# Kernel tuning notes

Measured on AMD Instinct MI355X. Metric: run time of the kernel, lower is better.

The kernel has to match this reference:

```python
import jax, jax.numpy as jnp
import numpy as np

DIM = 1024
NH = 16
HD = DIM // NH  # 64
NT = max(1, int(NH * 0.25))  # 4 time heads
NS = NH - NT                 # 12 space heads
SCALE = HD ** (-0.5)


def setup_inputs() -> dict:
    key = jax.random.key(0)
    ks = jax.random.split(key, 8)
    B, T = 2, 2048
    init = 0.02
    return {
        "x": jax.random.normal(ks[0], (B, T, DIM), dtype=jnp.float32),
        # weights stored as (in, out); torch Linear y = x @ W.T is equivalent
        "Wqt": jax.random.normal(ks[1], (DIM, NT * HD), dtype=jnp.float32) * init,
        "Wkt": jax.random.normal(ks[2], (DIM, NT * HD), dtype=jnp.float32) * init,
        "Wqs": jax.random.normal(ks[3], (DIM, NS * HD), dtype=jnp.float32) * init,
        "Wks": jax.random.normal(ks[4], (DIM, NS * HD), dtype=jnp.float32) * init,
        "Wv": jax.random.normal(ks[5], (DIM, DIM), dtype=jnp.float32) * init,
        "Wout": jax.random.normal(ks[6], (DIM, DIM), dtype=jnp.float32) * init,
        "bout": jnp.zeros((DIM,), dtype=jnp.float32),
        "w_sigma": jnp.zeros((1,), dtype=jnp.float32),
    }


def reference(x, Wqt, Wkt, Wqs, Wks, Wv, Wout, bout, w_sigma):
    B, T, D = x.shape
    Qt = (x @ Wqt).reshape(B, T, NT, HD)
    Kt = (x @ Wkt).reshape(B, T, NT, HD)
    Qs = (x @ Wqs).reshape(B, T, NS, HD)
    Ks = (x @ Wks).reshape(B, T, NS, HD)
    st = jnp.einsum('bthd,bshd->bths', Qt, Kt)  # [B,T,NT,T]
    ss = jnp.einsum('bthd,bshd->bths', Qs, Ks)  # [B,T,NS,T]
    sig = jax.nn.sigmoid(w_sigma)  # shape (1,), broadcasts
    score = jnp.concatenate([-sig * st, ss], axis=2) * SCALE  # [B,T,NH,T]
    attn = jax.nn.softmax(score, axis=-1)
    V = (x @ Wv).reshape(B, T, NH, HD)
    ctx = jnp.einsum('bths,bshd->bthd', attn, V).reshape(B, T, D)
    return ctx @ Wout + bout
```

## Files before the change

### kernel.cpp

```cpp
#include <hip/hip_runtime.h>
#include <hip/hip_bf16.h>

typedef __bf16 bf16_t;
typedef __bf16 bf16x4 __attribute__((ext_vector_type(4)));
typedef __bf16 bf16x8 __attribute__((ext_vector_type(8)));
typedef float  f32x4  __attribute__((ext_vector_type(4)));

#define DIM     1024
#define NHEAD   16
#define HDIM    64
#define NTIME   4
#define TSEQ    2048
#define NBATCH  2
#define SCALE_F 0.125f
#define LOG2E   1.4426950408889634f

#define GLL(gp, lp) __builtin_amdgcn_global_load_lds( \
    (const __attribute__((address_space(1))) unsigned int*)(const void*)(gp), \
    (__attribute__((address_space(3))) unsigned int*)(void*)(lp), 16, 0, 0)

#define OFF_WQKVT 0UL
#define OFF_WOUTT (OFF_WQKVT + 3072UL*1024UL*2UL)
#define OFF_Q     (OFF_WOUTT + 1024UL*1024UL*2UL)
#define OFF_K     (OFF_Q  + 2UL*16UL*2048UL*64UL*2UL)
#define OFF_VT    (OFF_K  + 2UL*16UL*2048UL*64UL*2UL)
#define OFF_CTX   (OFF_VT + 2UL*16UL*2048UL*64UL*2UL)

__global__ void prep_all(const float* __restrict__ x,
                         const float* __restrict__ Wqt, const float* __restrict__ Wkt,
                         const float* __restrict__ Wqs, const float* __restrict__ Wks,
                         const float* __restrict__ Wv,  const float* __restrict__ Wout,
                         bf16_t* __restrict__ Xb, bf16_t* __restrict__ WqkvT,
                         bf16_t* __restrict__ WoutT) {
    __shared__ float T[64][65];
    const int bid = blockIdx.x;
    if (bid < 2048) {
        int i = bid * 256 + threadIdx.x;
        const float4* s = (const float4*)(x + (size_t)i * 8);
        float4 a = s[0], b2 = s[1];
        bf16x8 v;
        v[0] = (bf16_t)a.x;  v[1] = (bf16_t)a.y;  v[2] = (bf16_t)a.z;  v[3] = (bf16_t)a.w;
        v[4] = (bf16_t)b2.x; v[5] = (bf16_t)b2.y; v[6] = (bf16_t)b2.z; v[7] = (bf16_t)b2.w;
        *(bf16x8*)(Xb + (size_t)i * 8) = v;
        return;
    }
    const int tc = threadIdx.x & 63, tr = threadIdx.x >> 6;
    if (bid < 2816) {
        const int l = bid - 2048;
        const int n0 = (l % 48) * 64;
        const int k0 = (l / 48) * 64;
        const int region = n0 >> 10;
        const int cc = n0 & 1023;
        const int h = cc >> 6;
        const float* src; int ncols, col0;
        if (region == 2) { src = Wv; ncols = 1024; col0 = cc; }
        else if (h < NTIME) { src = (region == 0) ? Wqt : Wkt; ncols = NTIME * HDIM; col0 = h * HDIM; }
        else                { src = (region == 0) ? Wqs : Wks; ncols = (NHEAD - NTIME) * HDIM; col0 = (h - NTIME) * HDIM; }
#pragma unroll
        for (int i = 0; i < 16; ++i) {
            int kl = tr * 16 + i;
            T[kl][tc] = src[(size_t)(k0 + kl) * ncols + col0 + tc];
        }
        __syncthreads();
#pragma unroll
        for (int i = 0; i < 16; ++i) {
            int nl = tr * 16 + i;
            WqkvT[(size_t)(n0 + nl) * 1024 + k0 + tc] = (bf16_t)T[tc][nl];
        }
    } else {
        const int l = bid - 2816;
        const int n0 = (l % 16) * 64;
        const int k0 = (l / 16) * 64;
#pragma unroll
        for (int i = 0; i < 16; ++i) {
            int kl = tr * 16 + i;
            T[kl][tc] = Wout[(size_t)(k0 + kl) * 1024 + n0 + tc];
        }
        __syncthreads();
#pragma unroll
        for (int i = 0; i < 16; ++i) {
            int nl = tr * 16 + i;
            WoutT[(size_t)(n0 + nl) * 1024 + k0 + tc] = (bf16_t)T[tc][nl];
        }
    }
}

template<int MODE, int NB>
__global__ __launch_bounds__(256)
void gemm_bf16(const bf16_t* __restrict__ Ab, const bf16_t* __restrict__ Bt,
               bf16_t* __restrict__ Qb, bf16_t* __restrict__ Kb, bf16_t* __restrict__ Vt,
               float* __restrict__ Cout, const float* __restrict__ bias)
{
    __shared__ __align__(16) bf16_t As[128][64];
    __shared__ __align__(16) bf16_t Bs[128][64];

    const int cpx = gridDim.x >> 3;
    const int l = (blockIdx.x & 7) * cpx + (blockIdx.x >> 3);
    const int m0 = (l / NB) * 128, n0 = (l % NB) * 128;

    const int tid  = threadIdx.x;
    const int lane = tid & 63;
    const int wave = tid >> 6;
    const int wm = (wave >> 1) * 64, wn = (wave & 1) * 64;
    const int g = lane >> 4, lr = lane & 15;

    f32x4 acc[4][4];
#pragma unroll
    for (int i = 0; i < 4; ++i)
#pragma unroll
        for (int j = 0; j < 4; ++j) acc[i][j] = f32x4{0.f, 0.f, 0.f, 0.f};

    for (int k0 = 0; k0 < 1024; k0 += 64) {
        __syncthreads();
#pragma unroll
        for (int c = 0; c < 4; ++c) {
            int idx  = tid + c * 256;
            int row  = idx >> 3;
            int csrc = (idx & 7) ^ (row & 7);
            GLL(Ab + (size_t)(m0 + row) * 1024 + k0 + csrc * 8,
                (char*)&As[0][0] + (c * 256 + wave * 64) * 16);
            GLL(Bt + (size_t)(n0 + row) * 1024 + k0 + csrc * 8,
                (char*)&Bs[0][0] + (c * 256 + wave * 64) * 16);
        }
        __syncthreads();

#pragma unroll
        for (int kk = 0; kk < 2; ++kk) {
            bf16x8 afr[4], bfr[4];
#pragma unroll
            for (int f = 0; f < 4; ++f) {
                int ra = wm + f * 16 + lr;
                afr[f] = *(const bf16x8*)((const char*)&As[0][0] + ra * 128 + (((kk * 4 + g) ^ (ra & 7)) << 4));
                int rb = wn + f * 16 + lr;
                bfr[f] = *(const bf16x8*)((const char*)&Bs[0][0] + rb * 128 + (((kk * 4 + g) ^ (rb & 7)) << 4));
            }
#pragma unroll
            for (int fm = 0; fm < 4; ++fm)
#pragma unroll
                for (int fn = 0; fn < 4; ++fn)
                    acc[fm][fn] = __builtin_amdgcn_mfma_f32_16x16x32_bf16(bfr[fn], afr[fm], acc[fm][fn], 0, 0, 0);
        }
    }

    const int region = n0 >> 10;
#pragma unroll
    for (int fm = 0; fm < 4; ++fm) {
        const int m = m0 + wm + fm * 16 + lr;
        const int b = m >> 11, t = m & 2047;
        const int ts = (t & ~31) | (((t >> 2) & 3) << 3) | (((t >> 4) & 1) << 2) | (t & 3);
#pragma unroll
        for (int fn = 0; fn < 4; ++fn) {
            const int nb = n0 + wn + fn * 16 + g * 4;
            if constexpr (MODE == 1) {
                float4 bb = *(const float4*)(bias + nb);
                float4 v;
                v.x = acc[fm][fn][0] + bb.x;
                v.y = acc[fm][fn][1] + bb.y;
                v.z = acc[fm][fn][2] + bb.z;
                v.w = acc[fm][fn][3] + bb.w;
                *(float4*)(Cout + (size_t)m * DIM + nb) = v;
            } else {
                const int cc = nb & 1023;
                const int h = cc >> 6, d0 = cc & 63;
                const size_t bh = (size_t)(b * NHEAD + h);
                if (region == 2) {
#pragma unroll
                    for (int r = 0; r < 4; ++r)
                        Vt[(bh * HDIM + d0 + r) * TSEQ + ts] = (bf16_t)acc[fm][fn][r];
                } else {
                    bf16x4 w;
#pragma unroll
                    for (int r = 0; r < 4; ++r) w[r] = (bf16_t)acc[fm][fn][r];
                    bf16_t* dst = (region == 0) ? Qb : Kb;
                    *(bf16x4*)(dst + (bh * TSEQ + t) * HDIM + d0) = w;
                }
            }
        }
    }
}

__global__ __launch_bounds__(256, 2)
void attn_kernel(const bf16_t* __restrict__ Qb, const bf16_t* __restrict__ Kb,
                 const bf16_t* __restrict__ Vt, bf16_t* __restrict__ ctx,
                 const float* __restrict__ w_sigma)
{
    __shared__ __align__(16) bf16_t Ktile[4][64][64];
    __shared__ __align__(16) bf16_t Vtile[4][64][64];

    const int l    = ((blockIdx.x & 7) << 6) + (blockIdx.x >> 3);
    const int qc   = l & 15;
    const int bh   = l >> 4;
    const int h    = bh & 15;
    const int b    = bh >> 4;
    const int tid  = threadIdx.x;
    const int lane = tid & 63;
    const int wave = tid >> 6;
    const int g = lane >> 4, lr = lane & 15;
    const int q0 = qc * 128 + wave * 32;

    const float sig = 1.f / (1.f + __expf(-w_sigma[0]));
    const float fl2 = ((h < NTIME) ? (-sig * SCALE_F) : SCALE_F) * LOG2E;

    const bf16_t* Qp = Qb + (size_t)bh * TSEQ * HDIM;
    const bf16_t* Kp = Kb + (size_t)bh * TSEQ * HDIM;
    const bf16_t* Vp = Vt + (size_t)bh * HDIM * TSEQ;

    bf16x8 qa0 = *(const bf16x8*)(Qp + (size_t)(q0 + lr) * HDIM + g * 8);
    bf16x8 qa1 = *(const bf16x8*)(Qp + (size_t)(q0 + lr) * HDIM + 32 + g * 8);
    bf16x8 qb0 = *(const bf16x8*)(Qp + (size_t)(q0 + 16 + lr) * HDIM + g * 8);
    bf16x8 qb1 = *(const bf16x8*)(Qp + (size_t)(q0 + 16 + lr) * HDIM + 32 + g * 8);
#pragma unroll
    for (int e = 0; e < 8; ++e) {
        qa0[e] = (bf16_t)((float)qa0[e] * fl2);
        qa1[e] = (bf16_t)((float)qa1[e] * fl2);
        qb0[e] = (bf16_t)((float)qb0[e] * fl2);
        qb1[e] = (bf16_t)((float)qb1[e] * fl2);
    }

    f32x4 oA[4], oB[4];
#pragma unroll
    for (int n = 0; n < 4; ++n) { oA[n] = f32x4{0.f,0.f,0.f,0.f}; oB[n] = f32x4{0.f,0.f,0.f,0.f}; }
    float lpA = 0.f, lpB = 0.f;

    const int trow = tid >> 3;
    const int tcg  = tid & 7;

    auto stage = [&](int s0, int buf) {
#pragma unroll
        for (int j = 0; j < 2; ++j) {
            int kr = j * 32 + trow;
            GLL(Kp + (size_t)(s0 + kr) * HDIM + ((tcg ^ (kr & 7)) << 3),
                (char*)&Ktile[buf][0][0] + (j * 256 + wave * 64) * 16);
            int vr = j * 32 + trow;
            GLL(Vp + (size_t)vr * TSEQ + s0 + ((tcg ^ (vr & 7)) << 3),
                (char*)&Vtile[buf][0][0] + (j * 256 + wave * 64) * 16);
        }
    };

    auto compute = [&](const char* Kt, const char* Vc) {
        bf16x4 wA[4], wB[4];
        __builtin_amdgcn_s_setprio(1);
#pragma unroll
        for (int st = 0; st < 4; ++st) {
            const int srow = st * 16 + lr;
            const int rs7 = lr & 7;
            bf16x8 kb0 = *(const bf16x8*)(Kt + srow * 128 + ((g ^ rs7) << 4));
            bf16x8 kb1 = *(const bf16x8*)(Kt + srow * 128 + (((4 + g) ^ rs7) << 4));
            f32x4 zA = f32x4{0.f,0.f,0.f,0.f}, zB = f32x4{0.f,0.f,0.f,0.f};
            zA = __builtin_amdgcn_mfma_f32_16x16x32_bf16(kb0, qa0, zA, 0, 0, 0);
            zA = __builtin_amdgcn_mfma_f32_16x16x32_bf16(kb1, qa1, zA, 0, 0, 0);
            zB = __builtin_amdgcn_mfma_f32_16x16x32_bf16(kb0, qb0, zB, 0, 0, 0);
            zB = __builtin_amdgcn_mfma_f32_16x16x32_bf16(kb1, qb1, zB, 0, 0, 0);
            float a0 = __builtin_amdgcn_exp2f(zA[0]);
            float a1 = __builtin_amdgcn_exp2f(zA[1]);
            float a2 = __builtin_amdgcn_exp2f(zA[2]);
            float a3 = __builtin_amdgcn_exp2f(zA[3]);
            float b0 = __builtin_amdgcn_exp2f(zB[0]);
            float b1 = __builtin_amdgcn_exp2f(zB[1]);
            float b2 = __builtin_amdgcn_exp2f(zB[2]);
            float b3 = __builtin_amdgcn_exp2f(zB[3]);
            wA[st][0] = (bf16_t)a0; wA[st][1] = (bf16_t)a1; wA[st][2] = (bf16_t)a2; wA[st][3] = (bf16_t)a3;
            wB[st][0] = (bf16_t)b0; wB[st][1] = (bf16_t)b1; wB[st][2] = (bf16_t)b2; wB[st][3] = (bf16_t)b3;
            lpA += (a0 + a1) + (a2 + a3);
            lpB += (b0 + b1) + (b2 + b3);
        }
        __builtin_amdgcn_s_setprio(0);

        __builtin_amdgcn_s_setprio(1);
#pragma unroll
        for (int kc = 0; kc < 2; ++kc) {
            bf16x8 paA, paB;
#pragma unroll
            for (int e = 0; e < 4; ++e) {
                paA[e]     = wA[kc * 2][e];
                paA[e + 4] = wA[kc * 2 + 1][e];
                paB[e]     = wB[kc * 2][e];
                paB[e + 4] = wB[kc * 2 + 1][e];
            }
#pragma unroll
            for (int n = 0; n < 4; ++n) {
                const int row = n * 16 + lr;
                bf16x8 vb = *(const bf16x8*)(Vc + row * 128 + (((kc * 4 + g) ^ (row & 7)) << 4));
                oA[n] = __builtin_amdgcn_mfma_f32_16x16x32_bf16(vb, paA, oA[n], 0, 0, 0);
                oB[n] = __builtin_amdgcn_mfma_f32_16x16x32_bf16(vb, paB, oB[n], 0, 0, 0);
            }
        }
        __builtin_amdgcn_s_setprio(0);
    };

    stage(0, 0);
    stage(64, 1);

    for (int step = 0; step < 32; ++step) {
        if (step + 2 < 32) stage((step + 2) * 64, (step + 2) & 3);
        if (step < 30)       asm volatile("s_waitcnt vmcnt(8)" ::: "memory");
        else if (step == 30) asm volatile("s_waitcnt vmcnt(4)" ::: "memory");
        else                 asm volatile("s_waitcnt vmcnt(0)" ::: "memory");
        __builtin_amdgcn_s_barrier();
        __builtin_amdgcn_sched_barrier(0);
        const int buf = step & 3;
        compute((const char*)&Ktile[buf][0][0], (const char*)&Vtile[buf][0][0]);
    }

    float lfA = lpA, lfB = lpB;
    lfA += __shfl_xor(lfA, 16, 64);
    lfA += __shfl_xor(lfA, 32, 64);
    lfB += __shfl_xor(lfB, 16, 64);
    lfB += __shfl_xor(lfB, 32, 64);
    float liA = 1.f / lfA, liB = 1.f / lfB;

    const int tA = q0 + lr, tB = q0 + 16 + lr;
#pragma unroll
    for (int n = 0; n < 4; ++n) {
        bf16x4 wA, wB;
#pragma unroll
        for (int r = 0; r < 4; ++r) {
            wA[r] = (bf16_t)(oA[n][r] * liA);
            wB[r] = (bf16_t)(oB[n][r] * liB);
        }
        *(bf16x4*)(ctx + ((size_t)(b * TSEQ + tA)) * DIM + h * HDIM + n * 16 + g * 4) = wA;
        *(bf16x4*)(ctx + ((size_t)(b * TSEQ + tB)) * DIM + h * HDIM + n * 16 + g * 4) = wB;
    }
}

extern "C" void kernel_launch(void* const* d_in, const int* in_sizes, int n_in,
                              void* d_out, int out_size, void* d_ws, size_t ws_size,
                              hipStream_t stream) {
    const float* x    = (const float*)d_in[0];
    const float* Wqt  = (const float*)d_in[1];
    const float* Wkt  = (const float*)d_in[2];
    const float* Wqs  = (const float*)d_in[3];
    const float* Wks  = (const float*)d_in[4];
    const float* Wv   = (const float*)d_in[5];
    const float* Wout = (const float*)d_in[6];
    const float* bout = (const float*)d_in[7];
    const float* wsig = (const float*)d_in[8];
    (void)in_sizes; (void)n_in; (void)out_size; (void)ws_size;

    char* ws = (char*)d_ws;
    bf16_t* WqkvT = (bf16_t*)(ws + OFF_WQKVT);
    bf16_t* WoutT = (bf16_t*)(ws + OFF_WOUTT);
    bf16_t* Qb    = (bf16_t*)(ws + OFF_Q);
    bf16_t* Kb    = (bf16_t*)(ws + OFF_K);
    bf16_t* Vt    = (bf16_t*)(ws + OFF_VT);
    bf16_t* ctx   = (bf16_t*)(ws + OFF_CTX);
    bf16_t* Xb    = ctx;
    float*  out   = (float*)d_out;

    prep_all<<<3072, 256, 0, stream>>>(x, Wqt, Wkt, Wqs, Wks, Wv, Wout, Xb, WqkvT, WoutT);

    gemm_bf16<0, 24><<<768, 256, 0, stream>>>(Xb, WqkvT, Qb, Kb, Vt, nullptr, nullptr);

    attn_kernel<<<512, 256, 0, stream>>>(Qb, Kb, Vt, ctx, wsig);

    gemm_bf16<1, 8><<<256, 256, 0, stream>>>(ctx, WoutT, nullptr, nullptr, nullptr, out, bout);
}
```

Measured before the change: 115.5 us.

## Double-buffer GEMM LDS tiles and remap blocks so each XCD owns column tiles

The projection GEMM now uses two LDS buffers for the A and B tiles. It issues the global-to-LDS loads for the next k-step before running the MFMAs on the current one, which leaves one barrier per iteration instead of two. The block-to-tile mapping also changes so each XCD gets a contiguous group of N-column tiles, which should improve reuse of weight rows in that XCD's L2. In exchange, LDS per block doubles to 64 KB, which can lower occupancy.

After: 118.2 us. 1.02x slower.

```diff
diff --git a/kernel.cpp b/kernel.cpp
--- a/kernel.cpp
+++ b/kernel.cpp
@@ -91,12 +91,14 @@
                bf16_t* __restrict__ Qb, bf16_t* __restrict__ Kb, bf16_t* __restrict__ Vt,
                float* __restrict__ Cout, const float* __restrict__ bias)
 {
-    __shared__ __align__(16) bf16_t As[128][64];
-    __shared__ __align__(16) bf16_t Bs[128][64];
-
-    const int cpx = gridDim.x >> 3;
-    const int l = (blockIdx.x & 7) * cpx + (blockIdx.x >> 3);
-    const int m0 = (l / NB) * 128, n0 = (l % NB) * 128;
+    __shared__ __align__(16) bf16_t As[2][128][64];
+    __shared__ __align__(16) bf16_t Bs[2][128][64];
+
+    constexpr int NXC = NB / 8;
+    const int xcd = blockIdx.x & 7;
+    const int r   = blockIdx.x >> 3;
+    const int m0 = (r / NXC) * 128;
+    const int n0 = (xcd * NXC + r % NXC) * 128;
 
     const int tid  = threadIdx.x;
     const int lane = tid & 63;
@@ -110,29 +112,37 @@
 #pragma unroll
         for (int j = 0; j < 4; ++j) acc[i][j] = f32x4{0.f, 0.f, 0.f, 0.f};
 
-    for (int k0 = 0; k0 < 1024; k0 += 64) {
-        __syncthreads();
+    auto stage = [&](int k0, int buf) {
 #pragma unroll
         for (int c = 0; c < 4; ++c) {
             int idx  = tid + c * 256;
             int row  = idx >> 3;
             int csrc = (idx & 7) ^ (row & 7);
             GLL(Ab + (size_t)(m0 + row) * 1024 + k0 + csrc * 8,
-                (char*)&As[0][0] + (c * 256 + wave * 64) * 16);
+                (char*)&As[buf][0][0] + (c * 256 + wave * 64) * 16);
             GLL(Bt + (size_t)(n0 + row) * 1024 + k0 + csrc * 8,
-                (char*)&Bs[0][0] + (c * 256 + wave * 64) * 16);
-        }
-        __syncthreads();
-
+                (char*)&Bs[buf][0][0] + (c * 256 + wave * 64) * 16);
+        }
+    };
+
+    stage(0, 0);
+    __syncthreads();
+
+    for (int t = 0; t < 16; ++t) {
+        const int buf = t & 1;
+        if (t < 15) stage((t + 1) * 64, buf ^ 1);
+
+        const char* Ac = (const char*)&As[buf][0][0];
+        const char* Bc = (const char*)&Bs[buf][0][0];
 #pragma unroll
         for (int kk = 0; kk < 2; ++kk) {
             bf16x8 afr[4], bfr[4];
 #pragma unroll
             for (int f = 0; f < 4; ++f) {
                 int ra = wm + f * 16 + lr;
-                afr[f] = *(const bf16x8*)((const char*)&As[0][0] + ra * 128 + (((kk * 4 + g) ^ (ra & 7)) << 4));
+                afr[f] = *(const bf16x8*)(Ac + ra * 128 + (((kk * 4 + g) ^ (ra & 7)) << 4));
                 int rb = wn + f * 16 + lr;
-                bfr[f] = *(const bf16x8*)((const char*)&Bs[0][0] + rb * 128 + (((kk * 4 + g) ^ (rb & 7)) << 4));
+                bfr[f] = *(const bf16x8*)(Bc + rb * 128 + (((kk * 4 + g) ^ (rb & 7)) << 4));
             }
 #pragma unroll
             for (int fm = 0; fm < 4; ++fm)
@@ -140,6 +150,7 @@
                 for (int fn = 0; fn < 4; ++fn)
                     acc[fm][fn] = __builtin_amdgcn_mfma_f32_16x16x32_bf16(bfr[fn], afr[fm], acc[fm][fn], 0, 0, 0);
         }
+        __syncthreads();
     }
 
     const int region = n0 >> 10;
@@ -165,12 +176,12 @@
                 const size_t bh = (size_t)(b * NHEAD + h);
                 if (region == 2) {
 #pragma unroll
-                    for (int r = 0; r < 4; ++r)
-                        Vt[(bh * HDIM + d0 + r) * TSEQ + ts] = (bf16_t)acc[fm][fn][r];
+                    for (int r2 = 0; r2 < 4; ++r2)
+                        Vt[(bh * HDIM + d0 + r2) * TSEQ + ts] = (bf16_t)acc[fm][fn][r2];
                 } else {
                     bf16x4 w;
 #pragma unroll
-                    for (int r = 0; r < 4; ++r) w[r] = (bf16_t)acc[fm][fn][r];
+                    for (int r2 = 0; r2 < 4; ++r2) w[r2] = (bf16_t)acc[fm][fn][r2];
                     bf16_t* dst = (region == 0) ? Qb : Kb;
                     *(bf16x4*)(dst + (bh * TSEQ + t) * HDIM + d0) = w;
                 }
```
